# Kernel optimization log

Hardware: AMD Instinct MI355X
Metric: run time of the kernel (lower is better)

## Reference

```python
import jax, jax.numpy as jnp
import numpy as np

B, T, C = 2, 2048, 2048
H, KVH, D = 16, 4, 128       # n_head, num_kv_heads, head_size
G = H // KVH                  # kv groups
SCALE = D ** -0.5
THETA = 10000.0


def setup_inputs() -> dict:
    key = jax.random.key(0)
    ks = jax.random.split(key, 5)
    s = 0.02
    return {
        "x": jax.random.normal(ks[0], (B, T, C), dtype=jnp.float32),
        "Wq": jax.random.normal(ks[1], (C, C), dtype=jnp.float32) * s,
        "bq": jnp.zeros((C,), jnp.float32),
        "Wk": jax.random.normal(ks[2], (C, KVH * D), dtype=jnp.float32) * s,
        "bk": jnp.zeros((KVH * D,), jnp.float32),
        "Wv": jax.random.normal(ks[3], (C, KVH * D), dtype=jnp.float32) * s,
        "bv": jnp.zeros((KVH * D,), jnp.float32),
        "Wo": jax.random.normal(ks[4], (C, C), dtype=jnp.float32) * s,
        "bo": jnp.zeros((C,), jnp.float32),
    }


def _rope(x):
    # x: [B, h, T, D]; interleaved-pair RoPE (lucidrains rotary-embedding-torch style)
    half = D // 2
    inv_freq = 1.0 / (THETA ** (jnp.arange(0, D, 2, dtype=jnp.float32) / D))  # [half]
    t = jnp.arange(T, dtype=jnp.float32)
    ang = t[:, None] * inv_freq[None, :]                 # [T, half]
    cos = jnp.repeat(jnp.cos(ang), 2, axis=-1)           # [T, D]
    sin = jnp.repeat(jnp.sin(ang), 2, axis=-1)
    xp = x.reshape(*x.shape[:-1], half, 2)
    x_rot = jnp.stack([-xp[..., 1], xp[..., 0]], axis=-1).reshape(x.shape)
    return x * cos + x_rot * sin


def reference(x, Wq, bq, Wk, bk, Wv, bv, Wo, bo):
    # projections
    q = (x @ Wq + bq).reshape(B, T, H, D).transpose(0, 2, 1, 3)      # [B,H,T,D]
    k = (x @ Wk + bk).reshape(B, T, KVH, D).transpose(0, 2, 1, 3)    # [B,KVH,T,D]
    v = (x @ Wv + bv).reshape(B, T, KVH, D).transpose(0, 2, 1, 3)
    # RoPE pre-attention
    q = _rope(q)
    k = _rope(k)
    # GQA: group query heads against shared KV heads (no repeat materialization)
    qg = q.reshape(B, KVH, G, T, D)
    att = jnp.einsum("bhgtd,bhsd->bhgts", qg, k) * SCALE              # [B,KVH,G,T,T]
    causal = jnp.tril(jnp.ones((T, T), dtype=bool))
    att = jnp.where(causal, att, jnp.float32(-jnp.inf))
    att = jax.nn.softmax(att, axis=-1)
    y = jnp.einsum("bhgts,bhsd->bhgtd", att, v)                        # [B,KVH,G,T,D]
    y = y.reshape(B, H, T, D).transpose(0, 2, 1, 3).reshape(B, T, C)
    return y @ Wo + bo
```

## Files before the change

kernel.cpp:

```cpp
#include <hip/hip_runtime.h>
#include <hip/hip_bf16.h>

typedef __bf16 bf16;
typedef __attribute__((ext_vector_type(8))) __bf16 bf16x8;
typedef __attribute__((ext_vector_type(4))) float f32x4;

#define SCALE2 (0.08838834764831845f * 1.4426950408889634f)

__device__ inline void gload16(const bf16* g, bf16* l) {
  __builtin_amdgcn_global_load_lds((const __attribute__((address_space(1))) void*)g,
                                   (__attribute__((address_space(3))) void*)l, 16, 0, 0);
}

__global__ void cvt_kernel(const float* __restrict__ in, bf16* __restrict__ out, int n8) {
  int i = blockIdx.x * 256 + threadIdx.x;
  if (i >= n8) return;
  const float* p = in + (size_t)i * 8;
  float4 a = *(const float4*)p, b = *(const float4*)(p + 4);
  union { uint4 u; bf16 h[8]; } un;
  un.h[0] = (bf16)a.x; un.h[1] = (bf16)a.y; un.h[2] = (bf16)a.z; un.h[3] = (bf16)a.w;
  un.h[4] = (bf16)b.x; un.h[5] = (bf16)b.y; un.h[6] = (bf16)b.z; un.h[7] = (bf16)b.w;
  *(uint4*)(out + (size_t)i * 8) = un.u;
}

__global__ void concat_bias_kernel(const float* __restrict__ bq, const float* __restrict__ bk,
                                   const float* __restrict__ bv, float* __restrict__ o) {
  int i = blockIdx.x * 256 + threadIdx.x;
  if (i >= 3072) return;
  o[i] = (i < 2048) ? bq[i] : (i < 2560 ? bk[i - 2048] : bv[i - 2560]);
}

__global__ __launch_bounds__(256)
void transpose_cvt_kernel(const float* __restrict__ in, bf16* __restrict__ out, int K, int N) {
  __shared__ bf16 tile[64][72];
  int n0 = blockIdx.x * 64, k0 = blockIdx.y * 64;
  int t = threadIdx.x;
  int r8 = t >> 5, c2 = (t & 31) * 2;
#pragma unroll
  for (int it = 0; it < 8; it++) {
    int row = it * 8 + r8;
    float2 v = *(const float2*)(in + (size_t)(k0 + row) * N + n0 + c2);
    tile[row][c2] = (bf16)v.x;
    tile[row][c2 + 1] = (bf16)v.y;
  }
  __syncthreads();
  int r = t >> 3, c = (t & 7) * 8;
  int rot = t & 7;
#pragma unroll
  for (int it = 0; it < 2; it++) {
    int rr = it * 32 + r;
    union { uint4 u; bf16 h[8]; } un;
#pragma unroll
    for (int j = 0; j < 8; j++) {
      int jj = (j + rot) & 7;
      un.h[jj] = tile[c + jj][rr];
    }
    *(uint4*)(out + (size_t)(n0 + rr) * K + k0 + c) = un.u;
  }
}

__global__ __launch_bounds__(256)
void transpose_v_kernel(const bf16* __restrict__ qkv, bf16* __restrict__ vT) {
  __shared__ bf16 tile[64][72];
  int z = blockIdx.z;
  int b = z >> 2, kvh = z & 3;
  int d0 = blockIdx.y * 64;
  int t0 = blockIdx.x * 64;
  const bf16* in = qkv + (size_t)(b * 2048) * 3072 + 2560 + kvh * 128;
  int t = threadIdx.x;
  int r = t >> 3, c = (t & 7) * 8;
#pragma unroll
  for (int it = 0; it < 2; it++) {
    int rr = it * 32 + r;
    *(uint4*)&tile[rr][c] = *(const uint4*)(in + (size_t)(t0 + rr) * 3072 + d0 + c);
  }
  __syncthreads();
  int rot = t & 7;
#pragma unroll
  for (int it = 0; it < 2; it++) {
    int rr = it * 32 + r;
    union { uint4 u; bf16 h[8]; } un;
#pragma unroll
    for (int j = 0; j < 8; j++) {
      int jj = (j + rot) & 7;
      un.h[jj] = tile[c + jj][rr];
    }
    *(uint4*)(vT + (size_t)(z * 128 + d0 + rr) * 2048 + t0 + c) = un.u;
  }
}

__global__ void rope_table_kernel(float* __restrict__ cost, float* __restrict__ sint) {
  int idx = blockIdx.x * 256 + threadIdx.x;
  int t = idx >> 6, i = idx & 63;
  float inv = expf(-(float)i * (logf(10000.f) / 64.f));
  float ang = (float)t * inv;
  cost[idx] = cosf(ang);
  sint[idx] = sinf(ang);
}

__global__ void rope_apply_kernel(bf16* __restrict__ qkv, const float* __restrict__ cost,
                                  const float* __restrict__ sint) {
  int p = blockIdx.x * 256 + threadIdx.x;
  if (p >= 4096 * 320) return;
  int row = p / 320;
  int rc = p - row * 320;
  int e = rc * 8;
  int t = row & 2047;
  int i0 = (e & 127) >> 1;
  bf16* ptr = qkv + (size_t)row * 3072 + e;
  float4 cv = *(const float4*)(cost + t * 64 + i0);
  float4 sv = *(const float4*)(sint + t * 64 + i0);
  float c[4] = {cv.x, cv.y, cv.z, cv.w}, s[4] = {sv.x, sv.y, sv.z, sv.w};
  union { uint4 u; bf16 h[8]; } un;
  un.u = *(const uint4*)ptr;
#pragma unroll
  for (int j = 0; j < 4; j++) {
    float x0 = (float)un.h[2 * j], x1 = (float)un.h[2 * j + 1];
    un.h[2 * j]     = (bf16)(x0 * c[j] - x1 * s[j]);
    un.h[2 * j + 1] = (bf16)(x1 * c[j] + x0 * s[j]);
  }
  *(uint4*)ptr = un.u;
}

template <typename OutT>
__global__ __launch_bounds__(256)
void gemm_bias_kernel(const bf16* __restrict__ A, const bf16* __restrict__ Bt,
                      const float* __restrict__ bias, OutT* __restrict__ C,
                      int M, int N, int K, int lda, int ldc) {
  __shared__ bf16 As[2][128 * 32];
  __shared__ bf16 Bs[2][128 * 32];
  int tid = threadIdx.x;
  int wv = tid >> 6, l = tid & 63;
  int wr = wv >> 1, wc = wv & 1;
  int lr = l & 15, g = l >> 4;

  int bid = blockIdx.y * gridDim.x + blockIdx.x;
  int cpx = (gridDim.x * gridDim.y) >> 3;
  int swz = (bid & 7) * cpx + (bid >> 3);
  int m0 = (swz / gridDim.x) * 128, n0 = (swz % gridDim.x) * 128;

  auto stage = [&](int k0, int buf) {
#pragma unroll
    for (int i = 0; i < 2; i++) {
      int e = i * 256 + tid;
      int row = e >> 2, c = e & 3;
      int csrc = (c ^ ((row >> 1) & 3)) * 8;
      gload16(A + (size_t)(m0 + row) * lda + k0 + csrc, &As[buf][(size_t)e * 8]);
      gload16(Bt + (size_t)(n0 + row) * K + k0 + csrc, &Bs[buf][(size_t)e * 8]);
    }
  };

  f32x4 acc[4][4] = {};
  stage(0, 0);
  __syncthreads();
  int cur = 0;
  int cswz = (g ^ ((lr >> 1) & 3)) * 8;
  for (int k0 = 32; k0 <= K; k0 += 32) {
    if (k0 < K) stage(k0, cur ^ 1);
    bf16x8 a[4], b[4];
#pragma unroll
    for (int mi = 0; mi < 4; mi++)
      a[mi] = *(const bf16x8*)&As[cur][(size_t)(wr * 64 + mi * 16 + lr) * 32 + cswz];
#pragma unroll
    for (int nj = 0; nj < 4; nj++)
      b[nj] = *(const bf16x8*)&Bs[cur][(size_t)(wc * 64 + nj * 16 + lr) * 32 + cswz];
#pragma unroll
    for (int mi = 0; mi < 4; mi++)
#pragma unroll
      for (int nj = 0; nj < 4; nj++)
        acc[mi][nj] = __builtin_amdgcn_mfma_f32_16x16x32_bf16(a[mi], b[nj], acc[mi][nj], 0, 0, 0);
    __syncthreads();
    cur ^= 1;
  }
#pragma unroll
  for (int nj = 0; nj < 4; nj++) {
    int gc = n0 + wc * 64 + nj * 16 + lr;
    float bv = bias[gc];
#pragma unroll
    for (int mi = 0; mi < 4; mi++) {
      int gr = m0 + wr * 64 + mi * 16 + g * 4;
#pragma unroll
      for (int reg = 0; reg < 4; reg++)
        C[(size_t)(gr + reg) * ldc + gc] = (OutT)(acc[mi][nj][reg] + bv);
    }
  }
}

__global__ __launch_bounds__(256)
void attn_kernel(const bf16* __restrict__ qkv, const bf16* __restrict__ vT,
                 bf16* __restrict__ ybuf) {
  __shared__ bf16 Ks[2][64 * 128];
  __shared__ bf16 Vts[2][128 * 64];
  __shared__ bf16 Ps[4][16][72];

  int pair = blockIdx.x;
  int bh = blockIdx.y;
  int b = bh >> 4, h = bh & 15;
  int kvh = h >> 2;
  int tid = threadIdx.x, w = tid >> 6, l = tid & 63;
  int lr = l & 15, g = l >> 4, lk = g * 8;

  const bf16* kbase = qkv + (size_t)(b * 2048) * 3072 + 2048 + kvh * 128;
  const bf16* vtb   = vT + (size_t)(b * 4 + kvh) * 128 * 2048;
  f32x4 zero4 = {0.f, 0.f, 0.f, 0.f};

  auto stage = [&](int kv0, int buf) {
#pragma unroll
    for (int it = 0; it < 4; it++) {
      int cidx = it * 256 + tid;
      {
        int row = cidx >> 4, c = cidx & 15, csrc = c ^ (row & 7);
        gload16(kbase + (size_t)(kv0 + row) * 3072 + csrc * 8, &Ks[buf][(size_t)cidx * 8]);
      }
      {
        int row = cidx >> 3, c = cidx & 7, csrc = c ^ (row & 7);
        gload16(vtb + (size_t)row * 2048 + kv0 + csrc * 8, &Vts[buf][(size_t)cidx * 8]);
      }
    }
  };

  for (int half = 0; half < 2; half++) {
    int qt = half == 0 ? 31 - pair : pair;
    int q0 = qt * 64;

    const bf16* qbase = qkv + (size_t)(b * 2048 + q0 + w * 16 + lr) * 3072 + h * 128;
    bf16x8 qf[4];
#pragma unroll
    for (int kk = 0; kk < 4; kk++) qf[kk] = *(const bf16x8*)(qbase + kk * 32 + lk);

    float m_r = -1e30f, l_r = 0.f;
    f32x4 o_acc[8];
#pragma unroll
    for (int f = 0; f < 8; f++) o_acc[f] = zero4;

    stage(0, 0);
    __syncthreads();
    int cur = 0;

    for (int kvt = 0; kvt <= qt; kvt++) {
      if (kvt < qt) stage((kvt + 1) * 64, cur ^ 1);

      const bf16* ksCur = Ks[cur];
      f32x4 sa[4];
#pragma unroll
      for (int nj = 0; nj < 4; nj++) sa[nj] = zero4;
#pragma unroll
      for (int kk = 0; kk < 4; kk++) {
        int cmem = (kk * 4 + g) ^ (lr & 7);
#pragma unroll
        for (int nj = 0; nj < 4; nj++) {
          bf16x8 kf = *(const bf16x8*)&ksCur[(size_t)((nj * 16 + lr) * 16 + cmem) * 8];
          sa[nj] = __builtin_amdgcn_mfma_f32_16x16x32_bf16(kf, qf[kk], sa[nj], 0, 0, 0);
        }
      }

      bool diag = (kvt == qt);
      int qpos = w * 16 + lr;
      float p[4][4];
#pragma unroll
      for (int nj = 0; nj < 4; nj++)
#pragma unroll
        for (int rg = 0; rg < 4; rg++) {
          float s = sa[nj][rg] * SCALE2;
          if (diag && (nj * 16 + g * 4 + rg > qpos)) s = -1e30f;
          p[nj][rg] = s;
        }

      float a0 = fmaxf(fmaxf(p[0][0], p[0][1]), fmaxf(p[0][2], p[0][3]));
      float a1 = fmaxf(fmaxf(p[1][0], p[1][1]), fmaxf(p[1][2], p[1][3]));
      float a2 = fmaxf(fmaxf(p[2][0], p[2][1]), fmaxf(p[2][2], p[2][3]));
      float a3 = fmaxf(fmaxf(p[3][0], p[3][1]), fmaxf(p[3][2], p[3][3]));
      float mx = fmaxf(fmaxf(a0, a1), fmaxf(a2, a3));
      mx = fmaxf(mx, __shfl_xor(mx, 16));
      mx = fmaxf(mx, __shfl_xor(mx, 32));

      if (__any(mx > m_r + 8.0f)) {
        float mnew = fmaxf(m_r, mx);
        float sc = exp2f(m_r - mnew);
        l_r *= sc;
        m_r = mnew;
        float osc[4];
#pragma unroll
        for (int rg = 0; rg < 4; rg++) osc[rg] = __shfl(sc, g * 4 + rg);
#pragma unroll
        for (int f = 0; f < 8; f++)
#pragma unroll
          for (int rg = 0; rg < 4; rg++) o_acc[f][rg] *= osc[rg];
      }

#pragma unroll
      for (int nj = 0; nj < 4; nj++)
#pragma unroll
        for (int rg = 0; rg < 4; rg++) p[nj][rg] = exp2f(p[nj][rg] - m_r);
      float s0 = (p[0][0] + p[0][1]) + (p[0][2] + p[0][3]);
      float s1 = (p[1][0] + p[1][1]) + (p[1][2] + p[1][3]);
      float s2 = (p[2][0] + p[2][1]) + (p[2][2] + p[2][3]);
      float s3 = (p[3][0] + p[3][1]) + (p[3][2] + p[3][3]);
      float rs = (s0 + s1) + (s2 + s3);
      rs += __shfl_xor(rs, 16);
      rs += __shfl_xor(rs, 32);
      l_r += rs;

#pragma unroll
      for (int nj = 0; nj < 4; nj++) {
        union { uint2 u; bf16 hh[4]; } pw;
#pragma unroll
        for (int rg = 0; rg < 4; rg++) pw.hh[rg] = (bf16)p[nj][rg];
        *(uint2*)&Ps[w][lr][nj * 16 + g * 4] = pw.u;
      }
      asm volatile("s_waitcnt lgkmcnt(0)" ::: "memory");
      __builtin_amdgcn_sched_barrier(0);

      const bf16* vtCur = Vts[cur];
#pragma unroll
      for (int kk2 = 0; kk2 < 2; kk2++) {
        bf16x8 pf = *(const bf16x8*)&Ps[w][lr][kk2 * 32 + lk];
        int cmem = (kk2 * 4 + g) ^ (lr & 7);
#pragma unroll
        for (int f = 0; f < 8; f++) {
          bf16x8 vf = *(const bf16x8*)&vtCur[(size_t)((f * 16 + lr) * 8 + cmem) * 8];
          o_acc[f] = __builtin_amdgcn_mfma_f32_16x16x32_bf16(pf, vf, o_acc[f], 0, 0, 0);
        }
      }
      __syncthreads();
      cur ^= 1;
    }

    float linv[4];
#pragma unroll
    for (int rg = 0; rg < 4; rg++) linv[rg] = 1.0f / __shfl(l_r, g * 4 + rg);
    size_t orow = (size_t)(b * 2048 + q0 + w * 16);
#pragma unroll
    for (int rg = 0; rg < 4; rg++) {
      int r = g * 4 + rg;
#pragma unroll
      for (int f = 0; f < 8; f++) {
        float ov = o_acc[f][rg] * linv[rg];
        ybuf[(orow + r) * 2048 + h * 128 + f * 16 + lr] = (bf16)ov;
      }
    }
    __syncthreads();
  }
}

extern "C" void kernel_launch(void* const* d_in, const int* in_sizes, int n_in,
                              void* d_out, int out_size, void* d_ws, size_t ws_size,
                              hipStream_t stream) {
  const float* x  = (const float*)d_in[0];
  const float* Wq = (const float*)d_in[1];
  const float* bq = (const float*)d_in[2];
  const float* Wk = (const float*)d_in[3];
  const float* bk = (const float*)d_in[4];
  const float* Wv = (const float*)d_in[5];
  const float* bv = (const float*)d_in[6];
  const float* Wo = (const float*)d_in[7];
  const float* bo = (const float*)d_in[8];
  float* out = (float*)d_out;

  char* w = (char*)d_ws;
  auto alloc = [&](size_t bytes) { char* p = w; w += (bytes + 255) & ~(size_t)255; return p; };
  bf16*  xb    = (bf16*)alloc((size_t)4096 * 2048 * 2);
  bf16*  wqkvT = (bf16*)alloc((size_t)3072 * 2048 * 2);
  bf16*  qkv   = (bf16*)alloc((size_t)4096 * 3072 * 2);
  bf16*  vTg   = (bf16*)alloc((size_t)8 * 128 * 2048 * 2);
  float* bqkv  = (float*)alloc((size_t)3072 * 4);
  float* cost  = (float*)alloc((size_t)2048 * 64 * 4);
  float* sint  = (float*)alloc((size_t)2048 * 64 * 4);
  bf16*  ybuf  = xb;
  bf16*  woT   = wqkvT;

  cvt_kernel<<<4096, 256, 0, stream>>>(x, xb, 4096 * 2048 / 8);
  concat_bias_kernel<<<12, 256, 0, stream>>>(bq, bk, bv, bqkv);
  transpose_cvt_kernel<<<dim3(32, 32), 256, 0, stream>>>(Wq, wqkvT, 2048, 2048);
  transpose_cvt_kernel<<<dim3(8, 32), 256, 0, stream>>>(Wk, wqkvT + (size_t)2048 * 2048, 2048, 512);
  transpose_cvt_kernel<<<dim3(8, 32), 256, 0, stream>>>(Wv, wqkvT + (size_t)2560 * 2048, 2048, 512);
  rope_table_kernel<<<512, 256, 0, stream>>>(cost, sint);
  gemm_bias_kernel<bf16><<<dim3(24, 32), 256, 0, stream>>>(xb, wqkvT, bqkv, qkv, 4096, 3072, 2048, 2048, 3072);
  transpose_cvt_kernel<<<dim3(32, 32), 256, 0, stream>>>(Wo, woT, 2048, 2048);
  transpose_v_kernel<<<dim3(32, 2, 8), 256, 0, stream>>>(qkv, vTg);
  rope_apply_kernel<<<5120, 256, 0, stream>>>(qkv, cost, sint);
  attn_kernel<<<dim3(16, 32), 256, 0, stream>>>(qkv, vTg, ybuf);
  gemm_bias_kernel<float><<<dim3(16, 32), 256, 0, stream>>>(ybuf, woT, bo, out, 4096, 2048, 2048, 2048, 2048);
}
```

Baseline: 296.2 us.

## Process both causal query tiles concurrently in one 512-thread attention block

```diff
diff --git a/kernel.cpp b/kernel.cpp
--- a/kernel.cpp
+++ b/kernel.cpp
@@ -186,12 +186,12 @@
   }
 }
 
-__global__ __launch_bounds__(256)
+__global__ __launch_bounds__(512, 4)
 void attn_kernel(const bf16* __restrict__ qkv, const bf16* __restrict__ vT,
                  bf16* __restrict__ ybuf) {
-  __shared__ bf16 Ks[2][64 * 128];
+  __shared__ bf16 Ks[64 * 128];
   __shared__ bf16 Vts[2][128 * 64];
-  __shared__ bf16 Ps[4][16][72];
+  __shared__ bf16 Ps[8][16][72];
 
   int pair = blockIdx.x;
   int bh = blockIdx.y;
@@ -199,70 +199,82 @@
   int kvh = h >> 2;
   int tid = threadIdx.x, w = tid >> 6, l = tid & 63;
   int lr = l & 15, g = l >> 4, lk = g * 8;
+  int wl = w & 3, wg = w >> 2;
+  int qt = wg ? pair : 31 - pair;
+  int q0 = qt * 64;
+  int nt = 32 - pair;
 
   const bf16* kbase = qkv + (size_t)(b * 2048) * 3072 + 2048 + kvh * 128;
   const bf16* vtb   = vT + (size_t)(b * 4 + kvh) * 128 * 2048;
   f32x4 zero4 = {0.f, 0.f, 0.f, 0.f};
 
-  auto stage = [&](int kv0, int buf) {
-#pragma unroll
-    for (int it = 0; it < 4; it++) {
-      int cidx = it * 256 + tid;
-      {
-        int row = cidx >> 4, c = cidx & 15, csrc = c ^ (row & 7);
-        gload16(kbase + (size_t)(kv0 + row) * 3072 + csrc * 8, &Ks[buf][(size_t)cidx * 8]);
-      }
-      {
-        int row = cidx >> 3, c = cidx & 7, csrc = c ^ (row & 7);
-        gload16(vtb + (size_t)row * 2048 + kv0 + csrc * 8, &Vts[buf][(size_t)cidx * 8]);
-      }
+  auto stageK = [&](int kv0) {
+#pragma unroll
+    for (int it = 0; it < 2; it++) {
+      int cidx = it * 512 + tid;
+      int row = cidx >> 4, c = cidx & 15, csrc = c ^ (row & 7);
+      gload16(kbase + (size_t)(kv0 + row) * 3072 + csrc * 8, &Ks[(size_t)cidx * 8]);
     }
   };
-
-  for (int half = 0; half < 2; half++) {
-    int qt = half == 0 ? 31 - pair : pair;
-    int q0 = qt * 64;
-
-    const bf16* qbase = qkv + (size_t)(b * 2048 + q0 + w * 16 + lr) * 3072 + h * 128;
-    bf16x8 qf[4];
-#pragma unroll
-    for (int kk = 0; kk < 4; kk++) qf[kk] = *(const bf16x8*)(qbase + kk * 32 + lk);
-
-    float m_r = -1e30f, l_r = 0.f;
-    f32x4 o_acc[8];
-#pragma unroll
-    for (int f = 0; f < 8; f++) o_acc[f] = zero4;
-
-    stage(0, 0);
-    __syncthreads();
-    int cur = 0;
-
-    for (int kvt = 0; kvt <= qt; kvt++) {
-      if (kvt < qt) stage((kvt + 1) * 64, cur ^ 1);
-
-      const bf16* ksCur = Ks[cur];
-      f32x4 sa[4];
-#pragma unroll
-      for (int nj = 0; nj < 4; nj++) sa[nj] = zero4;
+  auto stageV = [&](int kv0, int buf) {
+#pragma unroll
+    for (int it = 0; it < 2; it++) {
+      int cidx = it * 512 + tid;
+      int row = cidx >> 3, c = cidx & 7, csrc = c ^ (row & 7);
+      gload16(vtb + (size_t)row * 2048 + kv0 + csrc * 8, &Vts[buf][(size_t)cidx * 8]);
+    }
+  };
+
+  const bf16* qbase = qkv + (size_t)(b * 2048 + q0 + wl * 16 + lr) * 3072 + h * 128;
+  bf16x8 qf[4];
+#pragma unroll
+  for (int kk = 0; kk < 4; kk++) qf[kk] = *(const bf16x8*)(qbase + kk * 32 + lk);
+
+  float m_r = -1e30f, l_r = 0.f;
+  f32x4 o_acc[8];
+#pragma unroll
+  for (int f = 0; f < 8; f++) o_acc[f] = zero4;
+
+  stageK(0);
+  stageV(0, 0);
+  __syncthreads();
+  int cur = 0;
+
+  for (int kvt = 0; kvt < nt; kvt++) {
+    int kv0 = kvt * 64;
+    bool act = (kvt <= qt);
+
+    f32x4 sa[4];
+#pragma unroll
+    for (int nj = 0; nj < 4; nj++) sa[nj] = zero4;
+    if (act) {
 #pragma unroll
       for (int kk = 0; kk < 4; kk++) {
         int cmem = (kk * 4 + g) ^ (lr & 7);
 #pragma unroll
         for (int nj = 0; nj < 4; nj++) {
-          bf16x8 kf = *(const bf16x8*)&ksCur[(size_t)((nj * 16 + lr) * 16 + cmem) * 8];
+          bf16x8 kf = *(const bf16x8*)&Ks[(size_t)((nj * 16 + lr) * 16 + cmem) * 8];
           sa[nj] = __builtin_amdgcn_mfma_f32_16x16x32_bf16(kf, qf[kk], sa[nj], 0, 0, 0);
         }
       }
-
+    }
+    __syncthreads();
+
+    if (kvt + 1 < nt) {
+      stageK(kv0 + 64);
+      stageV(kv0 + 64, cur ^ 1);
+    }
+
+    if (act) {
       bool diag = (kvt == qt);
-      int qpos = w * 16 + lr;
+      int qpos = q0 + wl * 16 + lr;
       float p[4][4];
 #pragma unroll
       for (int nj = 0; nj < 4; nj++)
 #pragma unroll
         for (int rg = 0; rg < 4; rg++) {
           float s = sa[nj][rg] * SCALE2;
-          if (diag && (nj * 16 + g * 4 + rg > qpos)) s = -1e30f;
+          if (diag && (kv0 + nj * 16 + g * 4 + rg > qpos)) s = -1e30f;
           p[nj][rg] = s;
         }
 
@@ -322,24 +334,23 @@
           o_acc[f] = __builtin_amdgcn_mfma_f32_16x16x32_bf16(pf, vf, o_acc[f], 0, 0, 0);
         }
       }
-      __syncthreads();
-      cur ^= 1;
-    }
-
-    float linv[4];
-#pragma unroll
-    for (int rg = 0; rg < 4; rg++) linv[rg] = 1.0f / __shfl(l_r, g * 4 + rg);
-    size_t orow = (size_t)(b * 2048 + q0 + w * 16);
-#pragma unroll
-    for (int rg = 0; rg < 4; rg++) {
-      int r = g * 4 + rg;
-#pragma unroll
-      for (int f = 0; f < 8; f++) {
-        float ov = o_acc[f][rg] * linv[rg];
-        ybuf[(orow + r) * 2048 + h * 128 + f * 16 + lr] = (bf16)ov;
-      }
     }
     __syncthreads();
+    cur ^= 1;
+  }
+
+  float linv[4];
+#pragma unroll
+  for (int rg = 0; rg < 4; rg++) linv[rg] = 1.0f / __shfl(l_r, g * 4 + rg);
+  size_t orow = (size_t)(b * 2048 + q0 + wl * 16);
+#pragma unroll
+  for (int rg = 0; rg < 4; rg++) {
+    int r = g * 4 + rg;
+#pragma unroll
+    for (int f = 0; f < 8; f++) {
+      float ov = o_acc[f][rg] * linv[rg];
+      ybuf[(orow + r) * 2048 + h * 128 + f * 16 + lr] = (bf16)ov;
+    }
   }
 }
 
@@ -379,6 +390,6 @@
   transpose_cvt_kernel<<<dim3(32, 32), 256, 0, stream>>>(Wo, woT, 2048, 2048);
   transpose_v_kernel<<<dim3(32, 2, 8), 256, 0, stream>>>(qkv, vTg);
   rope_apply_kernel<<<5120, 256, 0, stream>>>(qkv, cost, sint);
-  attn_kernel<<<dim3(16, 32), 256, 0, stream>>>(qkv, vTg, ybuf);
+  attn_kernel<<<dim3(16, 32), 512, 0, stream>>>(qkv, vTg, ybuf);
   gemm_bias_kernel<float><<<dim3(16, 32), 256, 0, stream>>>(ybuf, woT, bo, out, 4096, 2048, 2048, 2048, 2048);
 }
```

Measured after the change: 288.6 us. -2.6%, faster.
